# Optimization experiments

Hardware: AMD Instinct MI355X
Metric: run time of the kernel (lower is better)

The kernel has to match this reference:

```python
import jax, jax.numpy as jnp
import numpy as np

VOCAB = 50257
EMBED = 128
N_HOPS = 3
MAX_STORY_LEN = 50


def setup_inputs() -> dict:
    key = jax.random.key(0)
    ks = jax.random.split(key, 10)
    B, n, T_c, T_q = 64, 50, 20, 20
    stories = jax.random.randint(ks[0], (B, n, T_c), 0, VOCAB)
    questions = jax.random.randint(ks[1], (B, T_q), 0, VOCAB)
    stories_masks = jax.random.randint(ks[2], (B, n, T_c), 0, 2)
    # Embedding tables, N(0, 0.1), padding_idx=0 row zeroed (as in torch nn.Embedding padding_idx)
    def emb(k, rows):
        w = 0.1 * jax.random.normal(k, (rows, EMBED), dtype=jnp.float32)
        return w.at[0].set(0.0)
    W_A = emb(ks[3], VOCAB)
    W_B = emb(ks[4], VOCAB)
    W_C = emb(ks[5], VOCAB)
    W_AT = emb(ks[6], MAX_STORY_LEN + 1)
    W_CT = emb(ks[7], MAX_STORY_LEN + 1)
    # nn.Linear(embed, vocab): weight [vocab, embed], bias [vocab]
    lim = 1.0 / np.sqrt(EMBED)
    W_lin = jax.random.uniform(ks[8], (VOCAB, EMBED), minval=-lim, maxval=lim, dtype=jnp.float32)
    b_lin = jax.random.uniform(ks[9], (VOCAB,), minval=-lim, maxval=lim, dtype=jnp.float32)
    return {"stories": stories, "questions": questions, "stories_masks": stories_masks,
            "W_A": W_A, "W_B": W_B, "W_C": W_C, "W_AT": W_AT, "W_CT": W_CT,
            "W_lin": W_lin, "b_lin": b_lin}


def reference(stories, questions, stories_masks, W_A, W_B, W_C, W_AT, W_CT, W_lin, b_lin):
    B, n, T_c = stories.shape
    # temporal index: sentence i -> i+1 if it contains any real token (mask==0), else 0 (padding)
    word_len = (stories_masks == 0).sum(axis=2)                      # [B, n]
    te_idx = jnp.arange(1, n + 1)[None, :] * (word_len >= 1)         # [B, n]
    # question embedding (basic encoding: sum over tokens)
    u = W_B[questions].sum(axis=1)                                   # [B, d]
    # memories/contexts: embeddings are identical every hop, compute once
    m = W_A[stories].sum(axis=2) + W_AT[te_idx]                      # [B, n, d]
    c = W_C[stories].sum(axis=2) + W_CT[te_idx]                      # [B, n, d]
    for _ in range(N_HOPS):
        score = jnp.einsum('bnd,bd->bn', m, u)                       # [B, n]
        probs = jax.nn.softmax(score, axis=1)
        o = jnp.einsum('bnd,bn->bd', c, probs)                       # [B, d]
        u = u + o
    return u @ W_lin.T + b_lin                                       # [B, vocab]
```

## Files before the change

### kernel.cpp

```cpp
#include <hip/hip_runtime.h>
#include <hip/hip_bf16.h>

#define VOCAB 50257
#define EMBED 128
#define NSENT 50
#define TC 20
#define TQ 20
#define BATCH 64
#define NHOPS 3

typedef __bf16 bf16x8 __attribute__((ext_vector_type(8)));
typedef float  f32x4v __attribute__((ext_vector_type(4)));

__global__ void __launch_bounds__(256) k_embed(
    const int* __restrict__ stories, const int* __restrict__ masks,
    const int* __restrict__ questions,
    const float* __restrict__ W_A, const float* __restrict__ W_B,
    const float* __restrict__ W_C,
    const float* __restrict__ W_AT, const float* __restrict__ W_CT,
    float* __restrict__ ws_m, float* __restrict__ ws_c, float* __restrict__ ws_u)
{
    __shared__ float sred[8][128];
    const int blk = blockIdx.x;
    const int tid = threadIdx.x;
    const int grp = tid >> 5;
    const int gl  = tid & 31;

    if (blk < BATCH * NSENT) {
        const int b = blk / NSENT;
        const int i = blk % NSENT;
        const int* mrow = masks + (b * NSENT + i) * TC;
        int cnt = 0;
        #pragma unroll
        for (int t = 0; t < TC; t++) cnt += (mrow[t] == 0);
        const int te = (cnt >= 1) ? (i + 1) : 0;

        const int* srow = stories + (b * NSENT + i) * TC;
        const int table = grp >> 2;
        const int sub   = grp & 3;
        const float* T = table ? W_C : W_A;

        f32x4v acc = {0.f, 0.f, 0.f, 0.f};
        #pragma unroll
        for (int t = 0; t < 5; t++) {
            const int tok = srow[sub + t * 4];
            acc += *(const f32x4v*)(T + (long)tok * EMBED + gl * 4);
        }
        *(f32x4v*)&sred[grp][gl * 4] = acc;
        __syncthreads();

        const int tb = tid >> 7, d = tid & 127;
        const float* TT = tb ? W_CT : W_AT;
        float v = sred[tb * 4 + 0][d] + sred[tb * 4 + 1][d]
                + sred[tb * 4 + 2][d] + sred[tb * 4 + 3][d]
                + TT[te * EMBED + d];
        float* dst = tb ? ws_c : ws_m;
        dst[(b * NSENT + i) * EMBED + d] = v;
    } else {
        const int b = blk - BATCH * NSENT;
        f32x4v acc = {0.f, 0.f, 0.f, 0.f};
        for (int t = grp; t < TQ; t += 8) {
            const int tok = questions[b * TQ + t];
            acc += *(const f32x4v*)(W_B + (long)tok * EMBED + gl * 4);
        }
        *(f32x4v*)&sred[grp][gl * 4] = acc;
        __syncthreads();
        if (tid < EMBED) {
            float v = 0.f;
            #pragma unroll
            for (int g = 0; g < 8; g++) v += sred[g][tid];
            ws_u[b * EMBED + tid] = v;
        }
    }
}

__global__ void __launch_bounds__(256) k_hops(
    const float* __restrict__ ws_m, const float* __restrict__ ws_c,
    const float* __restrict__ ws_u, __bf16* __restrict__ ws_ubf)
{
    __shared__ float smc[2 * NSENT * EMBED];
    __shared__ float su[EMBED];
    __shared__ float sp[64];
    __shared__ float ssc[64];
    __shared__ float spo[2][EMBED];

    const int b = blockIdx.x;
    const int tid = threadIdx.x;

    const f32x4v* gm = (const f32x4v*)(ws_m + b * NSENT * EMBED);
    const f32x4v* gc = (const f32x4v*)(ws_c + b * NSENT * EMBED);
    f32x4v* s4 = (f32x4v*)smc;
    for (int idx = tid; idx < NSENT * EMBED / 4; idx += 256) {
        s4[idx] = gm[idx];
        s4[NSENT * EMBED / 4 + idx] = gc[idx];
    }
    if (tid < EMBED) su[tid] = ws_u[b * EMBED + tid];
    __syncthreads();

    const int wave = tid >> 6, lane = tid & 63;
    const int d128 = tid & 127, hf = tid >> 7;
    for (int hop = 0; hop < NHOPS; hop++) {
        for (int i = wave; i < NSENT; i += 4) {
            float s = smc[i * EMBED + lane] * su[lane]
                    + smc[i * EMBED + 64 + lane] * su[64 + lane];
            #pragma unroll
            for (int off = 32; off >= 1; off >>= 1) s += __shfl_xor(s, off);
            if (lane == 0) ssc[i] = s;
        }
        __syncthreads();
        if (tid < 64) {
            float v = (tid < NSENT) ? ssc[tid] : -1e30f;
            float mx = v;
            #pragma unroll
            for (int off = 32; off >= 1; off >>= 1) mx = fmaxf(mx, __shfl_xor(mx, off));
            float e = (tid < NSENT) ? expf(v - mx) : 0.f;
            float sum = e;
            #pragma unroll
            for (int off = 32; off >= 1; off >>= 1) sum += __shfl_xor(sum, off);
            sp[tid] = e / sum;
        }
        __syncthreads();
        {
            float o = 0.f;
            #pragma unroll
            for (int k = 0; k < 25; k++) {
                const int i = hf * 25 + k;
                o += smc[NSENT * EMBED + i * EMBED + d128] * sp[i];
            }
            spo[hf][d128] = o;
        }
        __syncthreads();
        if (tid < EMBED) su[tid] += spo[0][tid] + spo[1][tid];
        __syncthreads();
    }
    if (tid < EMBED) ws_ubf[b * EMBED + tid] = (__bf16)su[tid];
}

#define VT 128
__global__ void __launch_bounds__(256) k_out(
    const __bf16* __restrict__ u_bf, const float* __restrict__ W_lin,
    const float* __restrict__ b_lin, float* __restrict__ out)
{
    __shared__ float sT[64][VT + 1];

    const int tid  = threadIdx.x;
    const int wave = tid >> 6, lane = tid & 63;
    const int m    = lane & 15;
    const int quad = lane >> 4;
    const int vbase = blockIdx.x * VT + wave * 32;

    f32x4v acc[2][4] = {};

    #pragma unroll
    for (int kc = 0; kc < 4; kc++) {
        const int k0 = kc * 32 + quad * 8;
        bf16x8 wb[2];
        #pragma unroll
        for (int s = 0; s < 2; s++) {
            int v = vbase + s * 16 + m;
            int vc = (v < VOCAB) ? v : (VOCAB - 1);
            const float* wrow = W_lin + (long)vc * EMBED;
            f32x4v w0 = *(const f32x4v*)(wrow + k0);
            f32x4v w1 = *(const f32x4v*)(wrow + k0 + 4);
            wb[s][0] = (__bf16)w0[0]; wb[s][1] = (__bf16)w0[1];
            wb[s][2] = (__bf16)w0[2]; wb[s][3] = (__bf16)w0[3];
            wb[s][4] = (__bf16)w1[0]; wb[s][5] = (__bf16)w1[1];
            wb[s][6] = (__bf16)w1[2]; wb[s][7] = (__bf16)w1[3];
        }
        #pragma unroll
        for (int bt = 0; bt < 4; bt++) {
            bf16x8 ab = *(const bf16x8*)(u_bf + (bt * 16 + m) * EMBED + k0);
            acc[0][bt] = __builtin_amdgcn_mfma_f32_16x16x32_bf16(ab, wb[0], acc[0][bt], 0, 0, 0);
            acc[1][bt] = __builtin_amdgcn_mfma_f32_16x16x32_bf16(ab, wb[1], acc[1][bt], 0, 0, 0);
        }
    }

    #pragma unroll
    for (int s = 0; s < 2; s++)
        #pragma unroll
        for (int bt = 0; bt < 4; bt++)
            #pragma unroll
            for (int r = 0; r < 4; r++)
                sT[bt * 16 + quad * 4 + r][wave * 32 + s * 16 + m] = acc[s][bt][r];
    __syncthreads();

    const int col = tid & 127;
    const int bh  = tid >> 7;
    const int v   = blockIdx.x * VT + col;
    if (v < VOCAB) {
        const float bl = b_lin[v];
        #pragma unroll
        for (int it = 0; it < 32; it++) {
            const int bb = bh * 32 + it;
            __builtin_nontemporal_store(sT[bb][col] + bl, &out[(long)bb * VOCAB + v]);
        }
    }
}

extern "C" void kernel_launch(void* const* d_in, const int* in_sizes, int n_in,
                              void* d_out, int out_size, void* d_ws, size_t ws_size,
                              hipStream_t stream) {
    const int*   stories   = (const int*)d_in[0];
    const int*   questions = (const int*)d_in[1];
    const int*   masks     = (const int*)d_in[2];
    const float* W_A       = (const float*)d_in[3];
    const float* W_B       = (const float*)d_in[4];
    const float* W_C       = (const float*)d_in[5];
    const float* W_AT      = (const float*)d_in[6];
    const float* W_CT      = (const float*)d_in[7];
    const float* W_lin     = (const float*)d_in[8];
    const float* b_lin     = (const float*)d_in[9];
    float* out = (float*)d_out;

    float* ws    = (float*)d_ws;
    float* ws_m  = ws;
    float* ws_c  = ws + BATCH * NSENT * EMBED;
    float* ws_u  = ws + 2 * BATCH * NSENT * EMBED;
    __bf16* ws_ubf = (__bf16*)(ws + 2 * BATCH * NSENT * EMBED + BATCH * EMBED);

    k_embed<<<dim3(BATCH * NSENT + BATCH), dim3(256), 0, stream>>>(
        stories, masks, questions, W_A, W_B, W_C, W_AT, W_CT, ws_m, ws_c, ws_u);
    k_hops<<<dim3(BATCH), dim3(256), 0, stream>>>(ws_m, ws_c, ws_u, ws_ubf);
    k_out<<<dim3((VOCAB + VT - 1) / VT), dim3(256), 0, stream>>>(ws_ubf, W_lin, b_lin, out);
}
```

Before: 161.7 us.

## Fuse embed, hops and output GEMM into one persistent kernel with grid barriers

Merges the three kernels into a single persistent launch of 512 blocks that synchronise through global atomic counters. Each block does a share of the embedding gathers, then prefetches its W_lin tiles into registers while it waits for the hop stage. The first 64 blocks run the memory hops, and then every block computes its output tiles with MFMA and writes them directly to global memory without staging through LDS. This removes launch gaps and overlaps the W_lin loads with earlier stages. In exchange it relies on all 512 blocks being co-resident for the spin barriers, needs an extra memset, and the direct stores are less coalesced.

```diff
diff --git a/kernel.cpp b/kernel.cpp
--- a/kernel.cpp
+++ b/kernel.cpp
@@ -8,191 +8,230 @@
 #define TQ 20
 #define BATCH 64
 #define NHOPS 3
+#define GRID 512
+#define VT 64
+#define NTILE ((VOCAB + VT - 1) / VT)
+#define NUNIT (BATCH * NSENT + BATCH)
 
 typedef __bf16 bf16x8 __attribute__((ext_vector_type(8)));
 typedef float  f32x4v __attribute__((ext_vector_type(4)));
 
-__global__ void __launch_bounds__(256) k_embed(
+struct WTile { bf16x8 wb[4]; float bl; };
+
+__device__ __forceinline__ WTile load_wtile(
+    const float* __restrict__ W_lin, const float* __restrict__ b_lin,
+    int tile, int wave, int m, int quad)
+{
+    WTile wt;
+    const int v  = tile * VT + wave * 16 + m;
+    const int vc = (v < VOCAB) ? v : (VOCAB - 1);
+    const float* wrow = W_lin + (long)vc * EMBED;
+    #pragma unroll
+    for (int kc = 0; kc < 4; kc++) {
+        const int k0 = kc * 32 + quad * 8;
+        f32x4v w0 = *(const f32x4v*)(wrow + k0);
+        f32x4v w1 = *(const f32x4v*)(wrow + k0 + 4);
+        wt.wb[kc][0] = (__bf16)w0[0]; wt.wb[kc][1] = (__bf16)w0[1];
+        wt.wb[kc][2] = (__bf16)w0[2]; wt.wb[kc][3] = (__bf16)w0[3];
+        wt.wb[kc][4] = (__bf16)w1[0]; wt.wb[kc][5] = (__bf16)w1[1];
+        wt.wb[kc][6] = (__bf16)w1[2]; wt.wb[kc][7] = (__bf16)w1[3];
+    }
+    wt.bl = b_lin[vc];
+    return wt;
+}
+
+__global__ void __launch_bounds__(256) k_fused(
     const int* __restrict__ stories, const int* __restrict__ masks,
     const int* __restrict__ questions,
     const float* __restrict__ W_A, const float* __restrict__ W_B,
     const float* __restrict__ W_C,
     const float* __restrict__ W_AT, const float* __restrict__ W_CT,
-    float* __restrict__ ws_m, float* __restrict__ ws_c, float* __restrict__ ws_u)
+    const float* __restrict__ W_lin, const float* __restrict__ b_lin,
+    float* __restrict__ out, float* __restrict__ ws,
+    unsigned* __restrict__ cnt)
 {
-    __shared__ float sred[8][128];
-    const int blk = blockIdx.x;
-    const int tid = threadIdx.x;
-    const int grp = tid >> 5;
-    const int gl  = tid & 31;
-
-    if (blk < BATCH * NSENT) {
-        const int b = blk / NSENT;
-        const int i = blk % NSENT;
-        const int* mrow = masks + (b * NSENT + i) * TC;
-        int cnt = 0;
-        #pragma unroll
-        for (int t = 0; t < TC; t++) cnt += (mrow[t] == 0);
-        const int te = (cnt >= 1) ? (i + 1) : 0;
-
-        const int* srow = stories + (b * NSENT + i) * TC;
-        const int table = grp >> 2;
-        const int sub   = grp & 3;
-        const float* T = table ? W_C : W_A;
-
-        f32x4v acc = {0.f, 0.f, 0.f, 0.f};
-        #pragma unroll
-        for (int t = 0; t < 5; t++) {
-            const int tok = srow[sub + t * 4];
-            acc += *(const f32x4v*)(T + (long)tok * EMBED + gl * 4);
-        }
-        *(f32x4v*)&sred[grp][gl * 4] = acc;
+    __shared__ __align__(16) float lds[13312];
+
+    float*  ws_m   = ws;
+    float*  ws_c   = ws + BATCH * NSENT * EMBED;
+    float*  ws_u   = ws + 2 * BATCH * NSENT * EMBED;
+    __bf16* ws_ubf = (__bf16*)(ws_u + BATCH * EMBED);
+
+    const int tid  = threadIdx.x;
+    const int g    = blockIdx.x;
+    const int wave = tid >> 6, lane = tid & 63;
+    const int m    = lane & 15, quad = lane >> 4;
+
+    {
+        float (*sred)[128] = (float (*)[128])lds;
+        const int grp = tid >> 5, gl = tid & 31;
+        for (int unit = g; unit < NUNIT; unit += GRID) {
+            if (unit < BATCH * NSENT) {
+                const int b = unit / NSENT, i = unit % NSENT;
+                const int* mrow = masks + (b * NSENT + i) * TC;
+                int c0 = 0;
+                #pragma unroll
+                for (int t = 0; t < TC; t++) c0 += (mrow[t] == 0);
+                const int te = (c0 >= 1) ? (i + 1) : 0;
+
+                const int* srow = stories + (b * NSENT + i) * TC;
+                const int table = grp >> 2, sub = grp & 3;
+                const float* T = table ? W_C : W_A;
+                f32x4v acc = {0.f, 0.f, 0.f, 0.f};
+                #pragma unroll
+                for (int t = 0; t < 5; t++) {
+                    const int tok = srow[sub + t * 4];
+                    acc += *(const f32x4v*)(T + (long)tok * EMBED + gl * 4);
+                }
+                *(f32x4v*)&sred[grp][gl * 4] = acc;
+                __syncthreads();
+                const int tb = tid >> 7, d = tid & 127;
+                const float* TT = tb ? W_CT : W_AT;
+                float v = sred[tb * 4 + 0][d] + sred[tb * 4 + 1][d]
+                        + sred[tb * 4 + 2][d] + sred[tb * 4 + 3][d]
+                        + TT[te * EMBED + d];
+                (tb ? ws_c : ws_m)[(b * NSENT + i) * EMBED + d] = v;
+                __syncthreads();
+            } else {
+                const int b = unit - BATCH * NSENT;
+                f32x4v acc = {0.f, 0.f, 0.f, 0.f};
+                for (int t = grp; t < TQ; t += 8) {
+                    const int tok = questions[b * TQ + t];
+                    acc += *(const f32x4v*)(W_B + (long)tok * EMBED + gl * 4);
+                }
+                *(f32x4v*)&sred[grp][gl * 4] = acc;
+                __syncthreads();
+                if (tid < EMBED) {
+                    float v = 0.f;
+                    #pragma unroll
+                    for (int gg = 0; gg < 8; gg++) v += sred[gg][tid];
+                    ws_u[b * EMBED + tid] = v;
+                }
+                __syncthreads();
+            }
+        }
+    }
+    __threadfence();
+    if (tid == 0) atomicAdd(&cnt[0], 1u);
+
+    WTile w0 = load_wtile(W_lin, b_lin, g, wave, m, quad);
+    const int t1 = g + GRID;
+    const bool has1 = (t1 < NTILE);
+    WTile w1 = {};
+    if (has1) w1 = load_wtile(W_lin, b_lin, t1, wave, m, quad);
+
+    if (g < BATCH) {
+        if (tid == 0) {
+            while (__hip_atomic_load(&cnt[0], __ATOMIC_RELAXED,
+                                     __HIP_MEMORY_SCOPE_AGENT) < GRID)
+                __builtin_amdgcn_s_sleep(1);
+        }
         __syncthreads();
-
-        const int tb = tid >> 7, d = tid & 127;
-        const float* TT = tb ? W_CT : W_AT;
-        float v = sred[tb * 4 + 0][d] + sred[tb * 4 + 1][d]
-                + sred[tb * 4 + 2][d] + sred[tb * 4 + 3][d]
-                + TT[te * EMBED + d];
-        float* dst = tb ? ws_c : ws_m;
-        dst[(b * NSENT + i) * EMBED + d] = v;
-    } else {
-        const int b = blk - BATCH * NSENT;
-        f32x4v acc = {0.f, 0.f, 0.f, 0.f};
-        for (int t = grp; t < TQ; t += 8) {
-            const int tok = questions[b * TQ + t];
-            acc += *(const f32x4v*)(W_B + (long)tok * EMBED + gl * 4);
-        }
-        *(f32x4v*)&sred[grp][gl * 4] = acc;
+        __threadfence();
+
+        float* smc = lds;
+        float* su  = lds + 12800;
+        float* sp  = lds + 12928;
+        float* ssc = lds + 12992;
+        float (*spo)[EMBED] = (float (*)[EMBED])(lds + 13056);
+
+        const f32x4v* gm = (const f32x4v*)(ws_m + g * NSENT * EMBED);
+        const f32x4v* gc = (const f32x4v*)(ws_c + g * NSENT * EMBED);
+        f32x4v* s4 = (f32x4v*)smc;
+        for (int idx = tid; idx < NSENT * EMBED / 4; idx += 256) {
+            s4[idx] = gm[idx];
+            s4[NSENT * EMBED / 4 + idx] = gc[idx];
+        }
+        if (tid < EMBED) su[tid] = ws_u[g * EMBED + tid];
         __syncthreads();
-        if (tid < EMBED) {
-            float v = 0.f;
-            #pragma unroll
-            for (int g = 0; g < 8; g++) v += sred[g][tid];
-            ws_u[b * EMBED + tid] = v;
-        }
-    }
-}
-
-__global__ void __launch_bounds__(256) k_hops(
-    const float* __restrict__ ws_m, const float* __restrict__ ws_c,
-    const float* __restrict__ ws_u, __bf16* __restrict__ ws_ubf)
-{
-    __shared__ float smc[2 * NSENT * EMBED];
-    __shared__ float su[EMBED];
-    __shared__ float sp[64];
-    __shared__ float ssc[64];
-    __shared__ float spo[2][EMBED];
-
-    const int b = blockIdx.x;
-    const int tid = threadIdx.x;
-
-    const f32x4v* gm = (const f32x4v*)(ws_m + b * NSENT * EMBED);
-    const f32x4v* gc = (const f32x4v*)(ws_c + b * NSENT * EMBED);
-    f32x4v* s4 = (f32x4v*)smc;
-    for (int idx = tid; idx < NSENT * EMBED / 4; idx += 256) {
-        s4[idx] = gm[idx];
-        s4[NSENT * EMBED / 4 + idx] = gc[idx];
-    }
-    if (tid < EMBED) su[tid] = ws_u[b * EMBED + tid];
+
+        const int d128 = tid & 127, hf = tid >> 7;
+        for (int hop = 0; hop < NHOPS; hop++) {
+            for (int i = wave; i < NSENT; i += 4) {
+                float s = smc[i * EMBED + lane] * su[lane]
+                        + smc[i * EMBED + 64 + lane] * su[64 + lane];
+                #pragma unroll
+                for (int off = 32; off >= 1; off >>= 1) s += __shfl_xor(s, off);
+                if (lane == 0) ssc[i] = s;
+            }
+            __syncthreads();
+            if (tid < 64) {
+                float v = (tid < NSENT) ? ssc[tid] : -1e30f;
+                float mx = v;
+                #pragma unroll
+                for (int off = 32; off >= 1; off >>= 1) mx = fmaxf(mx, __shfl_xor(mx, off));
+                float e = (tid < NSENT) ? expf(v - mx) : 0.f;
+                float sum = e;
+                #pragma unroll
+                for (int off = 32; off >= 1; off >>= 1) sum += __shfl_xor(sum, off);
+                sp[tid] = e / sum;
+            }
+            __syncthreads();
+            {
+                float o = 0.f;
+                #pragma unroll
+                for (int k = 0; k < 25; k++) {
+                    const int i = hf * 25 + k;
+                    o += smc[NSENT * EMBED + i * EMBED + d128] * sp[i];
+                }
+                spo[hf][d128] = o;
+            }
+            __syncthreads();
+            if (tid < EMBED) su[tid] += spo[0][tid] + spo[1][tid];
+            __syncthreads();
+        }
+        if (tid < EMBED) ws_ubf[g * EMBED + tid] = (__bf16)su[tid];
+        __syncthreads();
+        __threadfence();
+        if (tid == 0) atomicAdd(&cnt[1], 1u);
+    }
+
+    if (tid == 0) {
+        while (__hip_atomic_load(&cnt[1], __ATOMIC_RELAXED,
+                                 __HIP_MEMORY_SCOPE_AGENT) < BATCH)
+            __builtin_amdgcn_s_sleep(1);
+    }
     __syncthreads();
-
-    const int wave = tid >> 6, lane = tid & 63;
-    const int d128 = tid & 127, hf = tid >> 7;
-    for (int hop = 0; hop < NHOPS; hop++) {
-        for (int i = wave; i < NSENT; i += 4) {
-            float s = smc[i * EMBED + lane] * su[lane]
-                    + smc[i * EMBED + 64 + lane] * su[64 + lane];
-            #pragma unroll
-            for (int off = 32; off >= 1; off >>= 1) s += __shfl_xor(s, off);
-            if (lane == 0) ssc[i] = s;
-        }
-        __syncthreads();
-        if (tid < 64) {
-            float v = (tid < NSENT) ? ssc[tid] : -1e30f;
-            float mx = v;
-            #pragma unroll
-            for (int off = 32; off >= 1; off >>= 1) mx = fmaxf(mx, __shfl_xor(mx, off));
-            float e = (tid < NSENT) ? expf(v - mx) : 0.f;
-            float sum = e;
-            #pragma unroll
-            for (int off = 32; off >= 1; off >>= 1) sum += __shfl_xor(sum, off);
-            sp[tid] = e / sum;
-        }
-        __syncthreads();
-        {
-            float o = 0.f;
-            #pragma unroll
-            for (int k = 0; k < 25; k++) {
-                const int i = hf * 25 + k;
-                o += smc[NSENT * EMBED + i * EMBED + d128] * sp[i];
-            }
-            spo[hf][d128] = o;
-        }
-        __syncthreads();
-        if (tid < EMBED) su[tid] += spo[0][tid] + spo[1][tid];
-        __syncthreads();
-    }
-    if (tid < EMBED) ws_ubf[b * EMBED + tid] = (__bf16)su[tid];
-}
-
-#define VT 128
-__global__ void __launch_bounds__(256) k_out(
-    const __bf16* __restrict__ u_bf, const float* __restrict__ W_lin,
-    const float* __restrict__ b_lin, float* __restrict__ out)
-{
-    __shared__ float sT[64][VT + 1];
-
-    const int tid  = threadIdx.x;
-    const int wave = tid >> 6, lane = tid & 63;
-    const int m    = lane & 15;
-    const int quad = lane >> 4;
-    const int vbase = blockIdx.x * VT + wave * 32;
-
-    f32x4v acc[2][4] = {};
-
+    __threadfence();
+
+    bf16x8 ab[4][4];
     #pragma unroll
     for (int kc = 0; kc < 4; kc++) {
         const int k0 = kc * 32 + quad * 8;
-        bf16x8 wb[2];
-        #pragma unroll
-        for (int s = 0; s < 2; s++) {
-            int v = vbase + s * 16 + m;
-            int vc = (v < VOCAB) ? v : (VOCAB - 1);
-            const float* wrow = W_lin + (long)vc * EMBED;
-            f32x4v w0 = *(const f32x4v*)(wrow + k0);
-            f32x4v w1 = *(const f32x4v*)(wrow + k0 + 4);
-            wb[s][0] = (__bf16)w0[0]; wb[s][1] = (__bf16)w0[1];
-            wb[s][2] = (__bf16)w0[2]; wb[s][3] = (__bf16)w0[3];
-            wb[s][4] = (__bf16)w1[0]; wb[s][5] = (__bf16)w1[1];
-            wb[s][6] = (__bf16)w1[2]; wb[s][7] = (__bf16)w1[3];
-        }
-        #pragma unroll
-        for (int bt = 0; bt < 4; bt++) {
-            bf16x8 ab = *(const bf16x8*)(u_bf + (bt * 16 + m) * EMBED + k0);
-            acc[0][bt] = __builtin_amdgcn_mfma_f32_16x16x32_bf16(ab, wb[0], acc[0][bt], 0, 0, 0);
-            acc[1][bt] = __builtin_amdgcn_mfma_f32_16x16x32_bf16(ab, wb[1], acc[1][bt], 0, 0, 0);
-        }
-    }
-
-    #pragma unroll
-    for (int s = 0; s < 2; s++)
         #pragma unroll
         for (int bt = 0; bt < 4; bt++)
-            #pragma unroll
-            for (int r = 0; r < 4; r++)
-                sT[bt * 16 + quad * 4 + r][wave * 32 + s * 16 + m] = acc[s][bt][r];
-    __syncthreads();
-
-    const int col = tid & 127;
-    const int bh  = tid >> 7;
-    const int v   = blockIdx.x * VT + col;
-    if (v < VOCAB) {
-        const float bl = b_lin[v];
+            ab[kc][bt] = *(const bf16x8*)(ws_ubf + (bt * 16 + m) * EMBED + k0);
+    }
+    {
+        f32x4v acc[4] = {};
         #pragma unroll
-        for (int it = 0; it < 32; it++) {
-            const int bb = bh * 32 + it;
-            __builtin_nontemporal_store(sT[bb][col] + bl, &out[(long)bb * VOCAB + v]);
+        for (int kc = 0; kc < 4; kc++)
+            #pragma unroll
+            for (int bt = 0; bt < 4; bt++)
+                acc[bt] = __builtin_amdgcn_mfma_f32_16x16x32_bf16(ab[kc][bt], w0.wb[kc], acc[bt], 0, 0, 0);
+        const int v = g * VT + wave * 16 + m;
+        if (v < VOCAB) {
+            #pragma unroll
+            for (int bt = 0; bt < 4; bt++)
+                #pragma unroll
+                for (int r = 0; r < 4; r++)
+                    out[(long)(bt * 16 + quad * 4 + r) * VOCAB + v] = acc[bt][r] + w0.bl;
+        }
+    }
+    if (has1) {
+        f32x4v acc[4] = {};
+        #pragma unroll
+        for (int kc = 0; kc < 4; kc++)
+            #pragma unroll
+            for (int bt = 0; bt < 4; bt++)
+                acc[bt] = __builtin_amdgcn_mfma_f32_16x16x32_bf16(ab[kc][bt], w1.wb[kc], acc[bt], 0, 0, 0);
+        const int v = t1 * VT + wave * 16 + m;
+        if (v < VOCAB) {
+            #pragma unroll
+            for (int bt = 0; bt < 4; bt++)
+                #pragma unroll
+                for (int r = 0; r < 4; r++)
+                    out[(long)(bt * 16 + quad * 4 + r) * VOCAB + v] = acc[bt][r] + w1.bl;
         }
     }
 }
@@ -211,15 +250,11 @@
     const float* W_lin     = (const float*)d_in[8];
     const float* b_lin     = (const float*)d_in[9];
     float* out = (float*)d_out;
-
-    float* ws    = (float*)d_ws;
-    float* ws_m  = ws;
-    float* ws_c  = ws + BATCH * NSENT * EMBED;
-    float* ws_u  = ws + 2 * BATCH * NSENT * EMBED;
-    __bf16* ws_ubf = (__bf16*)(ws + 2 * BATCH * NSENT * EMBED + BATCH * EMBED);
-
-    k_embed<<<dim3(BATCH * NSENT + BATCH), dim3(256), 0, stream>>>(
-        stories, masks, questions, W_A, W_B, W_C, W_AT, W_CT, ws_m, ws_c, ws_u);
-    k_hops<<<dim3(BATCH), dim3(256), 0, stream>>>(ws_m, ws_c, ws_u, ws_ubf);
-    k_out<<<dim3((VOCAB + VT - 1) / VT), dim3(256), 0, stream>>>(ws_ubf, W_lin, b_lin, out);
+    float* ws  = (float*)d_ws;
+    unsigned* cnt = (unsigned*)((char*)d_ws + (32u << 20));
+
+    hipMemsetAsync(cnt, 0, 2 * sizeof(unsigned), stream);
+    k_fused<<<dim3(GRID), dim3(256), 0, stream>>>(
+        stories, masks, questions, W_A, W_B, W_C, W_AT, W_CT,
+        W_lin, b_lin, out, ws, cnt);
 }
```

New measurement: 288.0 us. +78.1%, slower.
